# Kernel tuning notes

Measured on AMD Instinct MI355X. Metric: run time of the kernel, lower is better.

## Reference

```python
import jax, jax.numpy as jnp
import numpy as np

MAX_DISP = 64


def setup_inputs() -> dict:
    key = jax.random.key(0)
    k1, k2 = jax.random.split(key)
    b, c, h, w = 4, 256, 180, 320
    left_feature = jax.random.normal(k1, (b, c, h, w), dtype=jnp.float32)
    right_feature = jax.random.normal(k2, (b, c, h, w), dtype=jnp.float32)
    return {"left_feature": left_feature, "right_feature": right_feature}


def reference(left_feature, right_feature):
    # Correlation cost volume: cost[:, i, :, x] = mean_c(left[:, :, :, x] * right[:, :, :, x - i])
    # for x >= i, else 0. Loop is over the small fixed disparity range (init arg).
    b, c, h, w = left_feature.shape
    slices = []
    for i in range(MAX_DISP):
        if i > 0:
            prod = jnp.mean(left_feature[:, :, :, i:] * right_feature[:, :, :, :-i], axis=1)  # [b, h, w-i]
            prod = jnp.pad(prod, ((0, 0), (0, 0), (i, 0)))  # zero-fill columns < i
        else:
            prod = jnp.mean(left_feature * right_feature, axis=1)  # [b, h, w]
        slices.append(prod)
    cost_volume = jnp.stack(slices, axis=1)  # [b, max_disp, h, w]
    return cost_volume
```

## Files before the change

### kernel.cpp

```cpp
#include <hip/hip_runtime.h>


#define Bb 4
#define Cc 256
#define Hh 180
#define Ww 320
#define MAXD 64
#define KC 16
#define NT 320
#define RSTRIDE 432
#define LSTRIDE 360

__device__ __forceinline__ int swz(int w) {
    int G = w >> 2;
    G = G + (G >> 3);
    return (G << 2) | (w & 3);
}

__global__ __launch_bounds__(NT, 4)
void _AA_CostVolume_63668595196248_kernel(const float* __restrict__ left,
                                          const float* __restrict__ right,
                                          float* __restrict__ out) {
    __shared__ float lds_r[KC][RSTRIDE];
    __shared__ float lds_l[KC][LSTRIDE];

    const int tid = threadIdx.x;
    const int bi  = blockIdx.x;
    const int b   = bi / Hh;
    const int h   = bi % Hh;

    const int threadi = tid & 7;
    const int threadx = tid >> 3;
    const int tx = threadx << 3;
    const int i0 = threadi << 3;

    if (tid < KC * 16) {
        const int row = tid >> 4;
        const int g4  = tid & 15;
        *(float4*)&lds_r[row][swz(g4 << 2)] = make_float4(0.f, 0.f, 0.f, 0.f);
    }

    int roff[4], loff[2];
    {
        const int p = 56 + tx - i0;
#pragma unroll
        for (int ii = 0; ii < 4; ++ii) roff[ii] = swz(p + (ii << 2));
#pragma unroll
        for (int ii = 0; ii < 2; ++ii) loff[ii] = swz(tx + (ii << 2));
    }

    const int tdiv = tid / 80;
    const int tmod = tid % 80;
    const int xcol = tmod << 2;
    const int rdst = swz(64 + xcol);
    const int ldst = swz(xcol);
    const int gbase = b * (Cc * Hh * Ww) + h * Ww + xcol;

    float acc[8][8];
#pragma unroll
    for (int di = 0; di < 8; ++di)
#pragma unroll
        for (int dx = 0; dx < 8; ++dx) acc[di][dx] = 0.f;

    for (int k0 = 0; k0 < Cc; k0 += KC) {
        __syncthreads();
#pragma unroll
        for (int u = 0; u < 4; ++u) {
            const int row = (u << 2) + tdiv;
            const int src = gbase + (k0 + row) * (Hh * Ww);
            const float4 rv = *(const float4*)(right + src);
            const float4 lv = *(const float4*)(left + src);
            *(float4*)&lds_r[row][rdst] = rv;
            *(float4*)&lds_l[row][ldst] = lv;
        }
        __syncthreads();

#pragma unroll 4
        for (int s = 0; s < KC; ++s) {
            const float* __restrict__ rr = lds_r[s];
            const float* __restrict__ lr = lds_l[s];
            float r[16], l[8];
#pragma unroll
            for (int ii = 0; ii < 4; ++ii)
                *(float4*)&r[ii << 2] = *(const float4*)&rr[roff[ii]];
#pragma unroll
            for (int ii = 0; ii < 2; ++ii)
                *(float4*)&l[ii << 2] = *(const float4*)&lr[loff[ii]];
#pragma unroll
            for (int di = 0; di < 8; ++di)
#pragma unroll
                for (int dx = 0; dx < 8; ++dx)
                    acc[di][dx] += l[dx] * r[8 + dx - di];
        }
    }

    const float scale = 1.0f / 256.0f;
#pragma unroll
    for (int di = 0; di < 8; ++di) {
        const int i = i0 + di;
        float v[8];
#pragma unroll
        for (int dx = 0; dx < 8; ++dx)
            v[dx] = (tx + dx >= i) ? acc[di][dx] * scale : 0.f;
        const int o = ((b * MAXD + i) * Hh + h) * Ww + tx;
        *(float4*)(out + o)     = make_float4(v[0], v[1], v[2], v[3]);
        *(float4*)(out + o + 4) = make_float4(v[4], v[5], v[6], v[7]);
    }
}

extern "C" void kernel_launch(void* const* d_in, const int* in_sizes, int n_in,
                              void* d_out, int out_size, void* d_ws, size_t ws_size,
                              hipStream_t stream) {
    const float* left  = (const float*)d_in[0];
    const float* right = (const float*)d_in[1];
    float* out = (float*)d_out;
    dim3 grid(Bb * Hh);
    dim3 block(NT);
    _AA_CostVolume_63668595196248_kernel<<<grid, block, 0, stream>>>(left, right, out);
}
```

Before: 534.3 us.

## Compute correlation with bf16 MFMA tiles instead of fp32 FMA outer products

Replaces the per-thread fp32 register-blocked outer product with bf16 MFMA 16x16x32 instructions. Each wave computes x-tiles against the band of shifted right-feature tiles. Inputs are converted to bf16 with round-to-nearest-even and stored as channel-pair packed words in LDS. Output is scattered from MFMA accumulator layout, and a separate pre-pass zeros the lower triangle. The aim is higher matrix throughput, at the cost of reduced precision, extra redundant tile products, and uncoalesced scalar output stores.

```diff
diff --git a/kernel.cpp b/kernel.cpp
--- a/kernel.cpp
+++ b/kernel.cpp
@@ -1,110 +1,129 @@
 #include <hip/hip_runtime.h>
 
+
+typedef short bf16x8 __attribute__((ext_vector_type(8)));
+typedef float f32x4 __attribute__((ext_vector_type(4)));
 
 #define Bb 4
 #define Cc 256
 #define Hh 180
 #define Ww 320
 #define MAXD 64
-#define KC 16
-#define NT 320
-#define RSTRIDE 432
-#define LSTRIDE 360
+#define KC 32
+#define NCHUNK (Cc / KC)
+#define RSTR 20
+#define HW (Hh * Ww)
 
-__device__ __forceinline__ int swz(int w) {
-    int G = w >> 2;
-    G = G + (G >> 3);
-    return (G << 2) | (w & 3);
+__device__ __forceinline__ unsigned int bf16rne2(float a, float b) {
+    unsigned int ua = __float_as_uint(a);
+    unsigned int ub = __float_as_uint(b);
+    ua = (ua + 0x7FFFu + ((ua >> 16) & 1u)) >> 16;
+    ub = (ub + 0x7FFFu + ((ub >> 16) & 1u)) & 0xFFFF0000u;
+    return ua | ub;
 }
 
-__global__ __launch_bounds__(NT, 4)
-void _AA_CostVolume_63668595196248_kernel(const float* __restrict__ left,
-                                          const float* __restrict__ right,
+__global__ __launch_bounds__(320, 3)
+void _AA_CostVolume_63668595196248_kernel(const float* __restrict__ L,
+                                          const float* __restrict__ R,
                                           float* __restrict__ out) {
-    __shared__ float lds_r[KC][RSTRIDE];
-    __shared__ float lds_l[KC][LSTRIDE];
+    __shared__ unsigned int sL[Ww * RSTR];
+    __shared__ unsigned int sR[Ww * RSTR];
 
     const int tid = threadIdx.x;
     const int bi  = blockIdx.x;
     const int b   = bi / Hh;
     const int h   = bi % Hh;
 
-    const int threadi = tid & 7;
-    const int threadx = tid >> 3;
-    const int tx = threadx << 3;
-    const int i0 = threadi << 3;
-
-    if (tid < KC * 16) {
-        const int row = tid >> 4;
-        const int g4  = tid & 15;
-        *(float4*)&lds_r[row][swz(g4 << 2)] = make_float4(0.f, 0.f, 0.f, 0.f);
+    {
+        const int ob = (b * MAXD * Hh + h) * Ww;
+        for (int z = tid; z < MAXD * MAXD; z += 320) {
+            const int i = z >> 6;
+            const int x = z & 63;
+            if (x < i) out[ob + i * HW + x] = 0.0f;
+        }
     }
 
-    int roff[4], loff[2];
-    {
-        const int p = 56 + tx - i0;
+    const int lane = tid & 63;
+    const int w    = tid >> 6;
+    const int q    = lane >> 4;
+    const int n    = lane & 15;
+
+    const int cp = tid & 15;
+    const int tq = tid >> 4;
+    const int inbase = (b * Cc + 2 * cp) * HW + h * Ww;
+
+    const int frag_off = n * RSTR + 4 * q;
+
+    f32x4 acc[4][5];
 #pragma unroll
-        for (int ii = 0; ii < 4; ++ii) roff[ii] = swz(p + (ii << 2));
+    for (int xt = 0; xt < 4; ++xt)
 #pragma unroll
-        for (int ii = 0; ii < 2; ++ii) loff[ii] = swz(tx + (ii << 2));
-    }
+        for (int du = 0; du < 5; ++du) {
+            f32x4 z = {0.f, 0.f, 0.f, 0.f};
+            acc[xt][du] = z;
+        }
 
-    const int tdiv = tid / 80;
-    const int tmod = tid % 80;
-    const int xcol = tmod << 2;
-    const int rdst = swz(64 + xcol);
-    const int ldst = swz(xcol);
-    const int gbase = b * (Cc * Hh * Ww) + h * Ww + xcol;
-
-    float acc[8][8];
+    for (int kc = 0; kc < NCHUNK; ++kc) {
+        __syncthreads();
+        const float* Lp = L + inbase + kc * KC * HW;
+        const float* Rp = R + inbase + kc * KC * HW;
 #pragma unroll
-    for (int di = 0; di < 8; ++di)
+        for (int s = 0; s < 4; ++s) {
+            const int xq = tq + 20 * s;
+            const float4 l0 = *(const float4*)(Lp + 4 * xq);
+            const float4 l1 = *(const float4*)(Lp + HW + 4 * xq);
+            const float4 r0 = *(const float4*)(Rp + 4 * xq);
+            const float4 r1 = *(const float4*)(Rp + HW + 4 * xq);
+            const float* l0f = (const float*)&l0;
+            const float* l1f = (const float*)&l1;
+            const float* r0f = (const float*)&r0;
+            const float* r1f = (const float*)&r1;
 #pragma unroll
-        for (int dx = 0; dx < 8; ++dx) acc[di][dx] = 0.f;
-
-    for (int k0 = 0; k0 < Cc; k0 += KC) {
-        __syncthreads();
-#pragma unroll
-        for (int u = 0; u < 4; ++u) {
-            const int row = (u << 2) + tdiv;
-            const int src = gbase + (k0 + row) * (Hh * Ww);
-            const float4 rv = *(const float4*)(right + src);
-            const float4 lv = *(const float4*)(left + src);
-            *(float4*)&lds_r[row][rdst] = rv;
-            *(float4*)&lds_l[row][ldst] = lv;
+            for (int j = 0; j < 4; ++j) {
+                sL[(4 * xq + j) * RSTR + cp] = bf16rne2(l0f[j], l1f[j]);
+                sR[(4 * xq + j) * RSTR + cp] = bf16rne2(r0f[j], r1f[j]);
+            }
         }
         __syncthreads();
 
-#pragma unroll 4
-        for (int s = 0; s < KC; ++s) {
-            const float* __restrict__ rr = lds_r[s];
-            const float* __restrict__ lr = lds_l[s];
-            float r[16], l[8];
+        bf16x8 af[4];
 #pragma unroll
-            for (int ii = 0; ii < 4; ++ii)
-                *(float4*)&r[ii << 2] = *(const float4*)&rr[roff[ii]];
+        for (int xt = 0; xt < 4; ++xt)
+            af[xt] = *(const bf16x8*)&sL[(16 * (4 * w + xt) + n) * RSTR + 4 * q];
+
 #pragma unroll
-            for (int ii = 0; ii < 2; ++ii)
-                *(float4*)&l[ii << 2] = *(const float4*)&lr[loff[ii]];
+        for (int uu = 0; uu < 8; ++uu) {
+            const int u = 4 * w + uu - 4;
+            if (u >= 0) {
+                const bf16x8 bfr = *(const bf16x8*)&sR[u * (16 * RSTR) + frag_off];
 #pragma unroll
-            for (int di = 0; di < 8; ++di)
-#pragma unroll
-                for (int dx = 0; dx < 8; ++dx)
-                    acc[di][dx] += l[dx] * r[8 + dx - di];
+                for (int xt = 0; xt < 4; ++xt) {
+                    const int du = xt - (uu - 4);
+                    if (du >= 0 && du <= 4)
+                        acc[xt][du] = __builtin_amdgcn_mfma_f32_16x16x32_bf16(
+                            af[xt], bfr, acc[xt][du], 0, 0, 0);
+                }
+            }
         }
     }
 
-    const float scale = 1.0f / 256.0f;
+    const float sc = 1.0f / 256.0f;
 #pragma unroll
-    for (int di = 0; di < 8; ++di) {
-        const int i = i0 + di;
-        float v[8];
+    for (int xt = 0; xt < 4; ++xt) {
+        const int t  = 4 * w + xt;
+        const int x0 = 16 * t + 4 * q;
 #pragma unroll
-        for (int dx = 0; dx < 8; ++dx)
-            v[dx] = (tx + dx >= i) ? acc[di][dx] * scale : 0.f;
-        const int o = ((b * MAXD + i) * Hh + h) * Ww + tx;
-        *(float4*)(out + o)     = make_float4(v[0], v[1], v[2], v[3]);
-        *(float4*)(out + o + 4) = make_float4(v[4], v[5], v[6], v[7]);
+        for (int du = 0; du < 5; ++du) {
+            if (t - du >= 0) {
+                const int ib = 16 * du + 4 * q - n;
+#pragma unroll
+                for (int r = 0; r < 4; ++r) {
+                    const int i = ib + r;
+                    if (i >= 0 && i < MAXD)
+                        out[((b * MAXD + i) * Hh + h) * Ww + x0 + r] = acc[xt][du][r] * sc;
+                }
+            }
+        }
     }
 }
 
@@ -115,6 +134,6 @@
     const float* right = (const float*)d_in[1];
     float* out = (float*)d_out;
     dim3 grid(Bb * Hh);
-    dim3 block(NT);
+    dim3 block(320);
     _AA_CostVolume_63668595196248_kernel<<<grid, block, 0, stream>>>(left, right, out);
 }
```

Result: faster. 503.1 us (-5.8%).
